# Performance work log

Measured on AMD Instinct MI355X. Metric: run time of the kernel, lower is better.

Reference implementation:

```python
import jax, jax.numpy as jnp
import numpy as np

N = 50000          # num nodes
E = 600000         # num edges
F_IN = 128         # num_features
H = 128            # graph_hidden_dim
R = 2              # num_relations
L = 3              # n_layers_conv
BN_EPS = 1e-5
BN_BETA = 1e-4     # BatchNorm bias init per module code


def setup_inputs() -> dict:
    key = jax.random.key(0)
    ks = jax.random.split(key, 9)
    s_in = 1.0 / np.sqrt(F_IN)
    s_h = 1.0 / np.sqrt(H)
    return {
        "x": jax.random.normal(ks[0], (N, F_IN), jnp.float32),
        "edge_index": jax.random.randint(ks[1], (2, E), 0, N, jnp.int32),
        "edge_type": jax.random.randint(ks[2], (E,), 0, R, jnp.int32),
        "W0_rel": jax.random.normal(ks[3], (R, F_IN, H), jnp.float32) * s_in,
        "W0_root": jax.random.normal(ks[4], (F_IN, H), jnp.float32) * s_in,
        "b0": jnp.zeros((H,), jnp.float32),
        "Ws_rel": jax.random.normal(ks[5], (L, R, H, H), jnp.float32) * s_h,
        "Ws_root": jax.random.normal(ks[6], (L, H, H), jnp.float32) * s_h,
        "bs": jnp.zeros((L, H), jnp.float32),
    }


def batchnorm(x):
    # training-mode BatchNorm1d over nodes; weight=1, bias=1e-4 (per init)
    mu = jnp.mean(x, axis=0)
    var = jnp.mean((x - mu) ** 2, axis=0)  # biased var, as torch uses for norm
    return (x - mu) * jax.lax.rsqrt(var + BN_EPS) + BN_BETA


def rgcn_conv(x, src, dst, edge_type, W_rel, W_root, b):
    # PyG RGCNConv, aggr='mean': per-relation mean of x[src] at dst,
    # then per-relation linear, plus root transform and bias.
    seg = dst * R + edge_type  # combined (node, relation) segment id
    msgs = x[src]                                   # [E, d] gather
    sums = jax.ops.segment_sum(msgs, seg, num_segments=N * R)
    cnts = jax.ops.segment_sum(jnp.ones((src.shape[0],), x.dtype), seg,
                               num_segments=N * R)
    mean = sums.reshape(N, R, -1) / jnp.maximum(cnts, 1.0).reshape(N, R, 1)
    out = jnp.einsum('nrd,rdh->nh', mean, W_rel) + x @ W_root + b
    return out


def reference(x, edge_index, edge_type, W0_rel, W0_root, b0, Ws_rel, Ws_root, bs):
    src, dst = edge_index[0], edge_index[1]
    h = batchnorm(x)
    h = jax.nn.relu(rgcn_conv(h, src, dst, edge_type, W0_rel, W0_root, b0))
    for i in range(L):
        h_ = batchnorm(h)
        h_ = jax.nn.relu(rgcn_conv(h_, src, dst, edge_type,
                                   Ws_rel[i], Ws_root[i], bs[i]))
        h = h + h_  # conv_residual=True
    return h  # gconv_dropout == 0
```

## Files before the change

kernel.cpp:

```cpp
#include <hip/hip_runtime.h>
#include <hip/hip_bf16.h>

#define N_NODES 50000
#define N_EDGES 600000
#define F 128
#define R 2
#define NLAYER 4
#define NSEG (N_NODES * R)
#define NSCB 98
#define KTOT 384
#define BN_EPS 1e-5f
#define BETA 1e-4f

typedef __hip_bfloat16 bf16;
typedef __attribute__((ext_vector_type(8))) short short8;
typedef __attribute__((ext_vector_type(4))) float floatx4;

__global__ void k_wt(const float* __restrict__ W0_rel, const float* __restrict__ W0_root,
                     const float* __restrict__ Ws_rel, const float* __restrict__ Ws_root,
                     bf16* __restrict__ Bt2) {
    int idx = blockIdx.x * 256 + threadIdx.x;
    if (idx >= NLAYER * F * KTOT) return;
    int l = idx / (F * KTOT);
    int rem = idx % (F * KTOT);
    int j = rem / KTOT, k = rem % KTOT;
    float v;
    if (k < 256) {
        int r = k >> 7, d = k & 127;
        v = (l == 0) ? W0_rel[((size_t)r * F + d) * F + j]
                     : Ws_rel[((size_t)((l - 1) * R + r) * F + d) * F + j];
    } else {
        int d = k - 256;
        v = (l == 0) ? W0_root[(size_t)d * F + j]
                     : Ws_root[((size_t)(l - 1) * F + d) * F + j];
    }
    Bt2[idx] = __float2bfloat16(v);
}

__global__ void k_count(const int* __restrict__ dst, const int* __restrict__ et,
                        int* __restrict__ cnt) {
    int e = blockIdx.x * 256 + threadIdx.x;
    if (e < N_EDGES) atomicAdd(&cnt[dst[e] * R + et[e]], 1);
}

__global__ void k_scan1(const int* __restrict__ cnt, int* __restrict__ off,
                        int* __restrict__ bsum) {
    int t = threadIdx.x;
    int g = blockIdx.x * 1024 + t;
    int v = (g < NSEG) ? cnt[g] : 0;
    int lane = t & 63;
    int wv = t >> 6;
    int x = v;
    for (int d = 1; d < 64; d <<= 1) {
        int y = __shfl_up(x, d, 64);
        if (lane >= d) x += y;
    }
    __shared__ int wtot[16];
    if (lane == 63) wtot[wv] = x;
    __syncthreads();
    if (t < 16) {
        int s = wtot[t];
        for (int d = 1; d < 16; d <<= 1) {
            int y = __shfl_up(s, d, 64);
            if (t >= d) s += y;
        }
        wtot[t] = s;
    }
    __syncthreads();
    int wpre = (wv == 0) ? 0 : wtot[wv - 1];
    int incl = x + wpre;
    if (g < NSEG) off[g] = incl - v;
    if (t == 1023) bsum[blockIdx.x] = incl;
}

__global__ void k_scan2(int* __restrict__ bsum) {
    __shared__ int s[128];
    int t = threadIdx.x;
    int v = (t < NSCB) ? bsum[t] : 0;
    s[t] = v;
    __syncthreads();
    for (int d = 1; d < 128; d <<= 1) {
        int y = (t >= d) ? s[t - d] : 0;
        __syncthreads();
        s[t] += y;
        __syncthreads();
    }
    if (t < NSCB) bsum[t] = s[t] - v;
}

__global__ void k_scan3(int* __restrict__ off, const int* __restrict__ bsum) {
    int g = blockIdx.x * 1024 + threadIdx.x;
    if (g < NSEG) off[g] += bsum[blockIdx.x];
}

__global__ void k_fill(const int* __restrict__ src, const int* __restrict__ dst,
                       const int* __restrict__ et, const int* __restrict__ off,
                       int* __restrict__ fill, int* __restrict__ esrc) {
    int e = blockIdx.x * 256 + threadIdx.x;
    if (e >= N_EDGES) return;
    int seg = dst[e] * R + et[e];
    int idx = off[seg] + atomicAdd(&fill[seg], 1);
    esrc[idx] = src[e];
}

__global__ void k_bnstats(const float* __restrict__ h, float* __restrict__ gs) {
    int c = threadIdx.x & 127;
    int rl = threadIdx.x >> 7;
    float s = 0.f, q = 0.f;
    for (int r = blockIdx.x * 2 + rl; r < N_NODES; r += gridDim.x * 2) {
        float v = h[(size_t)r * F + c];
        s += v; q += v * v;
    }
    __shared__ float ls[256], lq[256];
    ls[threadIdx.x] = s; lq[threadIdx.x] = q;
    __syncthreads();
    if (rl == 0) {
        atomicAdd(&gs[c], ls[c] + ls[c + 128]);
        atomicAdd(&gs[128 + c], lq[c] + lq[c + 128]);
    }
}

__global__ void k_bn(const float* __restrict__ hin, const float* __restrict__ gs,
                     bf16* __restrict__ hbn) {
    int idx = blockIdx.x * 256 + threadIdx.x;
    if (idx >= N_NODES * F / 4) return;
    int c4 = (idx * 4) & 127;
    float4 v = *(const float4*)(hin + (size_t)idx * 4);
    bf16 o[4];
    float vv[4] = {v.x, v.y, v.z, v.w};
    #pragma unroll
    for (int c = 0; c < 4; c++) {
        float mm = gs[c4 + c] * (1.0f / N_NODES);
        float qq = gs[128 + c4 + c] * (1.0f / N_NODES);
        float rs = rsqrtf(qq - mm * mm + BN_EPS);
        o[c] = __float2bfloat16((vv[c] - mm) * rs + BETA);
    }
    *(double*)(hbn + (size_t)idx * 4) = *(const double*)o;
}

__device__ __forceinline__ void seg_sum(const bf16* __restrict__ hb,
                                        const int* __restrict__ esrc,
                                        int o, int c, float& rx, float& ry) {
    float a0 = 0.f, a1 = 0.f, b0 = 0.f, b1 = 0.f;
    float e0 = 0.f, e1 = 0.f, d0 = 0.f, d1 = 0.f;
    int i = 0;
    for (; i + 4 <= c; i += 4) {
        int s0 = esrc[o + i], s1 = esrc[o + i + 1];
        int s2 = esrc[o + i + 2], s3 = esrc[o + i + 3];
        __hip_bfloat162 p0 = *(const __hip_bfloat162*)(hb + (size_t)s0 * F);
        __hip_bfloat162 p1 = *(const __hip_bfloat162*)(hb + (size_t)s1 * F);
        __hip_bfloat162 p2 = *(const __hip_bfloat162*)(hb + (size_t)s2 * F);
        __hip_bfloat162 p3 = *(const __hip_bfloat162*)(hb + (size_t)s3 * F);
        a0 += __bfloat162float(p0.x); a1 += __bfloat162float(p0.y);
        b0 += __bfloat162float(p1.x); b1 += __bfloat162float(p1.y);
        e0 += __bfloat162float(p2.x); e1 += __bfloat162float(p2.y);
        d0 += __bfloat162float(p3.x); d1 += __bfloat162float(p3.y);
    }
    for (; i < c; i++) {
        int sn = esrc[o + i];
        __hip_bfloat162 p = *(const __hip_bfloat162*)(hb + (size_t)sn * F);
        a0 += __bfloat162float(p.x); a1 += __bfloat162float(p.y);
    }
    rx = (a0 + b0) + (e0 + d0);
    ry = (a1 + b1) + (e1 + d1);
}

__global__ void k_agg(const bf16* __restrict__ hbn,
                      const int* __restrict__ cnt, const int* __restrict__ off,
                      const int* __restrict__ esrc, bf16* __restrict__ mm) {
    int wid = (blockIdx.x * 256 + threadIdx.x) >> 6;
    int lane = threadIdx.x & 63;
    if (wid >= N_NODES) return;
    int n = wid;
    int f = lane * 2;
    int2 cc = *(const int2*)(cnt + n * R);
    int c0 = cc.x, c1 = cc.y;
    int o0 = off[n * R];
    float inv0 = (c0 > 0) ? 1.0f / (float)c0 : 0.f;
    float inv1 = (c1 > 0) ? 1.0f / (float)c1 : 0.f;
    const bf16* hb = hbn + f;
    float s0x, s0y, s1x, s1y;
    seg_sum(hb, esrc, o0, c0, s0x, s0y);
    seg_sum(hb, esrc, o0 + c0, c1, s1x, s1y);
    __hip_bfloat162 w0, w1;
    w0.x = __float2bfloat16(s0x * inv0);
    w0.y = __float2bfloat16(s0y * inv0);
    w1.x = __float2bfloat16(s1x * inv1);
    w1.y = __float2bfloat16(s1y * inv1);
    *(__hip_bfloat162*)(mm + (size_t)n * 256 + f) = w0;
    *(__hip_bfloat162*)(mm + (size_t)n * 256 + 128 + f) = w1;
}

__launch_bounds__(512)
__global__ void k_gemm2(const bf16* __restrict__ mm, const bf16* __restrict__ hbn,
                        const bf16* __restrict__ Bt2, const float* __restrict__ bias,
                        float* __restrict__ h, float* __restrict__ outp, int layer) {
    __shared__ bf16 As[64 * 136];
    __shared__ bf16 Bs[128 * 136];
    int t = threadIdx.x;
    int m0 = blockIdx.x * 64;
    int w = t >> 6;
    int lane = t & 63;
    int msub = w & 3;
    int nh = w >> 2;
    int lm = lane & 15;
    int lq = lane >> 4;
    int m = m0 + msub * 16 + lm;
    floatx4 acc[4];
    #pragma unroll
    for (int j = 0; j < 4; j++) acc[j] = (floatx4){0.f, 0.f, 0.f, 0.f};
    for (int ci = 0; ci < 3; ci++) {
        __syncthreads();
        {
            for (int rr = 0; rr < 2; rr++) {
                int idx = rr * 512 + t;
                int row = idx >> 4;
                int kc = idx & 15;
                const bf16* srcp = (ci < 2)
                    ? (mm + (size_t)(m0 + row) * 256 + ci * 128 + kc * 8)
                    : (hbn + (size_t)(m0 + row) * F + kc * 8);
                *(short8*)(As + row * 136 + kc * 8) = *(const short8*)srcp;
            }
        }
        {
            for (int rr = 0; rr < 4; rr++) {
                int idx = rr * 512 + t;
                int row = idx >> 4;
                int kc = idx & 15;
                short8 v = *(const short8*)(Bt2 + (size_t)row * KTOT + ci * 128 + kc * 8);
                *(short8*)(Bs + row * 136 + kc * 8) = v;
            }
        }
        __syncthreads();
        short8 a[4];
        #pragma unroll
        for (int ki = 0; ki < 4; ki++)
            a[ki] = *(const short8*)(As + (msub * 16 + lm) * 136 + ki * 32 + lq * 8);
        for (int tt = 0; tt < 4; tt++) {
            int nt = nh * 4 + tt;
            short8 b[4];
            #pragma unroll
            for (int ki = 0; ki < 4; ki++)
                b[ki] = *(const short8*)(Bs + (nt * 16 + lm) * 136 + ki * 32 + lq * 8);
            #pragma unroll
            for (int ki = 0; ki < 4; ki++)
                acc[tt] = __builtin_amdgcn_mfma_f32_16x16x32_bf16(b[ki], a[ki], acc[tt], 0, 0, 0);
        }
    }
    if (m < N_NODES) {
        #pragma unroll
        for (int tt = 0; tt < 4; tt++) {
            int nt = nh * 4 + tt;
            int n0 = nt * 16 + lq * 4;
            float4 bv = *(const float4*)(bias + n0);
            float4 hv = {0.f, 0.f, 0.f, 0.f};
            if (layer > 0) hv = *(const float4*)(h + (size_t)m * F + n0);
            float4 o4;
            o4.x = fmaxf(acc[tt][0] + bv.x, 0.f) + hv.x;
            o4.y = fmaxf(acc[tt][1] + bv.y, 0.f) + hv.y;
            o4.z = fmaxf(acc[tt][2] + bv.z, 0.f) + hv.z;
            o4.w = fmaxf(acc[tt][3] + bv.w, 0.f) + hv.w;
            *(float4*)(h + (size_t)m * F + n0) = o4;
            if (outp) *(float4*)(outp + (size_t)m * F + n0) = o4;
        }
    }
}

extern "C" void kernel_launch(void* const* d_in, const int* in_sizes, int n_in,
                              void* d_out, int out_size, void* d_ws, size_t ws_size,
                              hipStream_t stream) {
    const float* x       = (const float*)d_in[0];
    const int*   eidx    = (const int*)d_in[1];
    const int*   etype   = (const int*)d_in[2];
    const float* W0_rel  = (const float*)d_in[3];
    const float* W0_root = (const float*)d_in[4];
    const float* b0      = (const float*)d_in[5];
    const float* Ws_rel  = (const float*)d_in[6];
    const float* Ws_root = (const float*)d_in[7];
    const float* bs      = (const float*)d_in[8];
    const int* src = eidx;
    const int* dst = eidx + N_EDGES;

    char* w = (char*)d_ws;
    float* h   = (float*)w; w += (size_t)N_NODES * F * 4;
    bf16*  hbn = (bf16*)w;  w += (size_t)N_NODES * F * 2;
    bf16*  mm  = (bf16*)w;  w += (size_t)N_NODES * 256 * 2;
    bf16*  Bt2 = (bf16*)w;  w += (size_t)NLAYER * F * KTOT * 2;
    int* cnt   = (int*)w;   w += (size_t)NSEG * 4;
    int* fill  = (int*)w;   w += (size_t)NSEG * 4;
    float* stats = (float*)w; w += (size_t)NLAYER * 256 * 4;
    int* off   = (int*)w;   w += (size_t)NSEG * 4;
    int* esrc  = (int*)w;   w += (size_t)N_EDGES * 4;
    int* bsum  = (int*)w;   w += 128 * 4;

    hipMemsetAsync(cnt, 0, (size_t)NSEG * 4 * 2 + (size_t)NLAYER * 256 * 4, stream);
    k_wt<<<(NLAYER * F * KTOT + 255) / 256, 256, 0, stream>>>(W0_rel, W0_root, Ws_rel, Ws_root, Bt2);
    k_count<<<(N_EDGES + 255) / 256, 256, 0, stream>>>(dst, etype, cnt);
    k_scan1<<<NSCB, 1024, 0, stream>>>(cnt, off, bsum);
    k_scan2<<<1, 128, 0, stream>>>(bsum);
    k_scan3<<<NSCB, 1024, 0, stream>>>(off, bsum);
    k_fill<<<(N_EDGES + 255) / 256, 256, 0, stream>>>(src, dst, etype, off, fill, esrc);

    for (int l = 0; l < NLAYER; l++) {
        float* gs = stats + l * 256;
        const float* bias = (l == 0) ? b0 : (bs + (size_t)(l - 1) * F);
        const float* hin = (l == 0) ? x : h;
        k_bnstats<<<512, 256, 0, stream>>>(hin, gs);
        k_bn<<<(N_NODES * F / 4 + 255) / 256, 256, 0, stream>>>(hin, gs, hbn);
        k_agg<<<(N_NODES * 64 + 255) / 256, 256, 0, stream>>>(hbn, cnt, off, esrc, mm);
        k_gemm2<<<(N_NODES + 63) / 64, 512, 0, stream>>>(
            mm, hbn, Bt2 + (size_t)l * F * KTOT, bias, h,
            (l == 3) ? (float*)d_out : nullptr, l);
    }
}
```

Before: 505.0 us.

## Fuse neighbor mean aggregation into the RGCN GEMM kernel

Merges the separate aggregation kernel into the GEMM kernel. Each wave aggregates 8 nodes' per-relation means into registers, and those values are written directly into the shared-memory A tile. This removes the intermediate mm buffer round trip through global memory and one kernel launch per layer. In exchange, the GEMM blocks now carry the irregular gather latency with fewer waves in flight (782 blocks of 512 threads). Register pressure also rises, and the per-edge weighting does extra FMAs on both relation accumulators.

```diff
diff --git a/kernel.cpp b/kernel.cpp
--- a/kernel.cpp
+++ b/kernel.cpp
@@ -138,69 +138,72 @@
     *(double*)(hbn + (size_t)idx * 4) = *(const double*)o;
 }
 
-__device__ __forceinline__ void seg_sum(const bf16* __restrict__ hb,
-                                        const int* __restrict__ esrc,
-                                        int o, int c, float& rx, float& ry) {
-    float a0 = 0.f, a1 = 0.f, b0 = 0.f, b1 = 0.f;
-    float e0 = 0.f, e1 = 0.f, d0 = 0.f, d1 = 0.f;
-    int i = 0;
-    for (; i + 4 <= c; i += 4) {
-        int s0 = esrc[o + i], s1 = esrc[o + i + 1];
-        int s2 = esrc[o + i + 2], s3 = esrc[o + i + 3];
-        __hip_bfloat162 p0 = *(const __hip_bfloat162*)(hb + (size_t)s0 * F);
-        __hip_bfloat162 p1 = *(const __hip_bfloat162*)(hb + (size_t)s1 * F);
-        __hip_bfloat162 p2 = *(const __hip_bfloat162*)(hb + (size_t)s2 * F);
-        __hip_bfloat162 p3 = *(const __hip_bfloat162*)(hb + (size_t)s3 * F);
-        a0 += __bfloat162float(p0.x); a1 += __bfloat162float(p0.y);
-        b0 += __bfloat162float(p1.x); b1 += __bfloat162float(p1.y);
-        e0 += __bfloat162float(p2.x); e1 += __bfloat162float(p2.y);
-        d0 += __bfloat162float(p3.x); d1 += __bfloat162float(p3.y);
-    }
-    for (; i < c; i++) {
-        int sn = esrc[o + i];
-        __hip_bfloat162 p = *(const __hip_bfloat162*)(hb + (size_t)sn * F);
-        a0 += __bfloat162float(p.x); a1 += __bfloat162float(p.y);
-    }
-    rx = (a0 + b0) + (e0 + d0);
-    ry = (a1 + b1) + (e1 + d1);
-}
-
-__global__ void k_agg(const bf16* __restrict__ hbn,
-                      const int* __restrict__ cnt, const int* __restrict__ off,
-                      const int* __restrict__ esrc, bf16* __restrict__ mm) {
-    int wid = (blockIdx.x * 256 + threadIdx.x) >> 6;
-    int lane = threadIdx.x & 63;
-    if (wid >= N_NODES) return;
-    int n = wid;
-    int f = lane * 2;
-    int2 cc = *(const int2*)(cnt + n * R);
-    int c0 = cc.x, c1 = cc.y;
-    int o0 = off[n * R];
-    float inv0 = (c0 > 0) ? 1.0f / (float)c0 : 0.f;
-    float inv1 = (c1 > 0) ? 1.0f / (float)c1 : 0.f;
-    const bf16* hb = hbn + f;
-    float s0x, s0y, s1x, s1y;
-    seg_sum(hb, esrc, o0, c0, s0x, s0y);
-    seg_sum(hb, esrc, o0 + c0, c1, s1x, s1y);
-    __hip_bfloat162 w0, w1;
-    w0.x = __float2bfloat16(s0x * inv0);
-    w0.y = __float2bfloat16(s0y * inv0);
-    w1.x = __float2bfloat16(s1x * inv1);
-    w1.y = __float2bfloat16(s1y * inv1);
-    *(__hip_bfloat162*)(mm + (size_t)n * 256 + f) = w0;
-    *(__hip_bfloat162*)(mm + (size_t)n * 256 + 128 + f) = w1;
-}
-
 __launch_bounds__(512)
-__global__ void k_gemm2(const bf16* __restrict__ mm, const bf16* __restrict__ hbn,
-                        const bf16* __restrict__ Bt2, const float* __restrict__ bias,
-                        float* __restrict__ h, float* __restrict__ outp, int layer) {
+__global__ void k_agg_gemm(const bf16* __restrict__ hbn,
+                           const int* __restrict__ cnt, const int* __restrict__ off,
+                           const int* __restrict__ esrc,
+                           const bf16* __restrict__ Bt2, const float* __restrict__ bias,
+                           float* __restrict__ h, float* __restrict__ outp, int layer) {
     __shared__ bf16 As[64 * 136];
     __shared__ bf16 Bs[128 * 136];
     int t = threadIdx.x;
     int m0 = blockIdx.x * 64;
     int w = t >> 6;
     int lane = t & 63;
+    int f = lane * 2;
+    const bf16* hb = hbn + f;
+    __hip_bfloat162 mm0r[8], mm1r[8];
+    #pragma unroll
+    for (int j = 0; j < 8; j++) {
+        int n = m0 + w * 8 + j;
+        float a0 = 0.f, a1 = 0.f, b0 = 0.f, b1 = 0.f;
+        if (n < N_NODES) {
+            int2 cc = *(const int2*)(cnt + n * R);
+            int c0 = cc.x, c1 = cc.y;
+            int o0 = off[n * R];
+            int ctot = c0 + c1;
+            float inv0 = (c0 > 0) ? 1.0f / (float)c0 : 0.f;
+            float inv1 = (c1 > 0) ? 1.0f / (float)c1 : 0.f;
+            float sxA[4], syA[4], sxB[4], syB[4];
+            #pragma unroll
+            for (int k = 0; k < 4; k++) { sxA[k] = 0.f; syA[k] = 0.f; sxB[k] = 0.f; syB[k] = 0.f; }
+            int i = 0;
+            for (; i + 4 <= ctot; i += 4) {
+                int sn[4];
+                #pragma unroll
+                for (int k = 0; k < 4; k++) sn[k] = esrc[o0 + i + k];
+                __hip_bfloat162 p[4];
+                #pragma unroll
+                for (int k = 0; k < 4; k++)
+                    p[k] = *(const __hip_bfloat162*)(hb + (size_t)sn[k] * F);
+                #pragma unroll
+                for (int k = 0; k < 4; k++) {
+                    float wa = (i + k < c0) ? inv0 : 0.f;
+                    float wb = (i + k < c0) ? 0.f : inv1;
+                    float px = __bfloat162float(p[k].x);
+                    float py = __bfloat162float(p[k].y);
+                    sxA[k] = fmaf(px, wa, sxA[k]); syA[k] = fmaf(py, wa, syA[k]);
+                    sxB[k] = fmaf(px, wb, sxB[k]); syB[k] = fmaf(py, wb, syB[k]);
+                }
+            }
+            for (; i < ctot; i++) {
+                int sn = esrc[o0 + i];
+                __hip_bfloat162 p = *(const __hip_bfloat162*)(hb + (size_t)sn * F);
+                float wa = (i < c0) ? inv0 : 0.f;
+                float wb = (i < c0) ? 0.f : inv1;
+                float px = __bfloat162float(p.x);
+                float py = __bfloat162float(p.y);
+                sxA[0] = fmaf(px, wa, sxA[0]); syA[0] = fmaf(py, wa, syA[0]);
+                sxB[0] = fmaf(px, wb, sxB[0]); syB[0] = fmaf(py, wb, syB[0]);
+            }
+            a0 = (sxA[0] + sxA[1]) + (sxA[2] + sxA[3]);
+            a1 = (syA[0] + syA[1]) + (syA[2] + syA[3]);
+            b0 = (sxB[0] + sxB[1]) + (sxB[2] + sxB[3]);
+            b1 = (syB[0] + syB[1]) + (syB[2] + syB[3]);
+        }
+        mm0r[j].x = __float2bfloat16(a0); mm0r[j].y = __float2bfloat16(a1);
+        mm1r[j].x = __float2bfloat16(b0); mm1r[j].y = __float2bfloat16(b1);
+    }
     int msub = w & 3;
     int nh = w >> 2;
     int lm = lane & 15;
@@ -211,25 +214,29 @@
     for (int j = 0; j < 4; j++) acc[j] = (floatx4){0.f, 0.f, 0.f, 0.f};
     for (int ci = 0; ci < 3; ci++) {
         __syncthreads();
-        {
+        if (ci < 2) {
+            #pragma unroll
+            for (int j = 0; j < 8; j++) {
+                int row = w * 8 + j;
+                *(__hip_bfloat162*)(As + row * 136 + f) = (ci == 0) ? mm0r[j] : mm1r[j];
+            }
+        } else {
             for (int rr = 0; rr < 2; rr++) {
                 int idx = rr * 512 + t;
                 int row = idx >> 4;
                 int kc = idx & 15;
-                const bf16* srcp = (ci < 2)
-                    ? (mm + (size_t)(m0 + row) * 256 + ci * 128 + kc * 8)
-                    : (hbn + (size_t)(m0 + row) * F + kc * 8);
-                *(short8*)(As + row * 136 + kc * 8) = *(const short8*)srcp;
+                short8 v = {0, 0, 0, 0, 0, 0, 0, 0};
+                if (m0 + row < N_NODES)
+                    v = *(const short8*)(hbn + (size_t)(m0 + row) * F + kc * 8);
+                *(short8*)(As + row * 136 + kc * 8) = v;
             }
         }
-        {
-            for (int rr = 0; rr < 4; rr++) {
-                int idx = rr * 512 + t;
-                int row = idx >> 4;
-                int kc = idx & 15;
-                short8 v = *(const short8*)(Bt2 + (size_t)row * KTOT + ci * 128 + kc * 8);
-                *(short8*)(Bs + row * 136 + kc * 8) = v;
-            }
+        for (int rr = 0; rr < 4; rr++) {
+            int idx = rr * 512 + t;
+            int row = idx >> 4;
+            int kc = idx & 15;
+            short8 v = *(const short8*)(Bt2 + (size_t)row * KTOT + ci * 128 + kc * 8);
+            *(short8*)(Bs + row * 136 + kc * 8) = v;
         }
         __syncthreads();
         short8 a[4];
@@ -284,7 +291,6 @@
     char* w = (char*)d_ws;
     float* h   = (float*)w; w += (size_t)N_NODES * F * 4;
     bf16*  hbn = (bf16*)w;  w += (size_t)N_NODES * F * 2;
-    bf16*  mm  = (bf16*)w;  w += (size_t)N_NODES * 256 * 2;
     bf16*  Bt2 = (bf16*)w;  w += (size_t)NLAYER * F * KTOT * 2;
     int* cnt   = (int*)w;   w += (size_t)NSEG * 4;
     int* fill  = (int*)w;   w += (size_t)NSEG * 4;
@@ -307,9 +313,8 @@
         const float* hin = (l == 0) ? x : h;
         k_bnstats<<<512, 256, 0, stream>>>(hin, gs);
         k_bn<<<(N_NODES * F / 4 + 255) / 256, 256, 0, stream>>>(hin, gs, hbn);
-        k_agg<<<(N_NODES * 64 + 255) / 256, 256, 0, stream>>>(hbn, cnt, off, esrc, mm);
-        k_gemm2<<<(N_NODES + 63) / 64, 512, 0, stream>>>(
-            mm, hbn, Bt2 + (size_t)l * F * KTOT, bias, h,
+        k_agg_gemm<<<(N_NODES + 63) / 64, 512, 0, stream>>>(
+            hbn, cnt, off, esrc, Bt2 + (size_t)l * F * KTOT, bias, h,
             (l == 3) ? (float*)d_out : nullptr, l);
     }
 }
```

Measured after the change: 563.7 us. 11.6% more time.
